# Kernel optimization log

Measured on AMD Instinct MI355X. Metric: run time of the kernel, lower is better.

The kernel has to match this reference:

```python
import jax, jax.numpy as jnp
import numpy as np

N = 20000
M = 32          # max_neighbors
IN_DIM = 256
OUT_DIM = 256
H = 4           # num_heads
D = OUT_DIM // H  # head_dim = 64
LN_EPS = 1e-5
NEG_INF = -1.0e9


def setup_inputs() -> dict:
    key = jax.random.key(0)
    ks = jax.random.split(key, 6)
    h = jax.random.normal(ks[0], (N, IN_DIM), dtype=jnp.float32)
    neighbor_idx = jax.random.randint(ks[1], (N, M), 0, N, dtype=jnp.int32)
    neighbor_mask = jax.random.randint(ks[2], (N, M), 0, 2, dtype=jnp.int32)
    # parameters (xavier-ish scaling)
    W = jax.random.normal(ks[3], (IN_DIM, OUT_DIM), dtype=jnp.float32) / np.sqrt(IN_DIM)
    a_l = jax.random.normal(ks[4], (H, D), dtype=jnp.float32) / np.sqrt(D)
    a_r = jax.random.normal(ks[5], (H, D), dtype=jnp.float32) / np.sqrt(D)
    ln_gamma = jnp.ones((OUT_DIM,), dtype=jnp.float32)
    ln_beta = jnp.zeros((OUT_DIM,), dtype=jnp.float32)
    return {"h": h, "neighbor_idx": neighbor_idx, "neighbor_mask": neighbor_mask,
            "W": W, "a_l": a_l, "a_r": a_r, "ln_gamma": ln_gamma, "ln_beta": ln_beta}


def reference(h, neighbor_idx, neighbor_mask, W, a_l, a_r, ln_gamma, ln_beta):
    h_proj = h @ W                                   # [N, OUT_DIM]
    h_heads = h_proj.reshape(N, H, D)                # [N, H, D]
    # per-node score halves; gathering scalars instead of full features for er
    el = jnp.einsum('nhd,hd->nh', h_heads, a_l)      # [N, H]
    er_node = jnp.einsum('nhd,hd->nh', h_heads, a_r) # [N, H]
    er = er_node[neighbor_idx]                       # [N, M, H]
    e = jax.nn.leaky_relu(el[:, None, :] + er, negative_slope=0.2)  # [N, M, H]
    e = jnp.where(neighbor_mask[:, :, None] == 0, NEG_INF, e)
    alpha = jax.nn.softmax(e, axis=1)                # softmax over neighbors
    neigh_h = h_heads[neighbor_idx]                  # [N, M, H, D]
    out_heads = jnp.einsum('nmh,nmhd->nhd', alpha, neigh_h)
    H_cat = out_heads.reshape(N, OUT_DIM)
    res = h_proj                                     # in_dim == out_dim -> res_proj is None
    out = jax.nn.gelu(H_cat + res, approximate=False)
    # LayerNorm over last dim
    mu = jnp.mean(out, axis=-1, keepdims=True)
    var = jnp.var(out, axis=-1, keepdims=True)
    out = (out - mu) * jax.lax.rsqrt(var + LN_EPS) * ln_gamma + ln_beta
    return out
```

## Files before the change

### kernel.cpp

```cpp
#include <hip/hip_runtime.h>
#include <math.h>

#define N_NODES 20000
#define M_NEI   32
#define DIM     256
#define H_HEADS 4
#define D_HEAD  64
#define LN_EPS  1e-5f
#define NEG_INF -1.0e9f
#define APAD    264

using short8  = __attribute__((ext_vector_type(8))) short;
using short4v = __attribute__((ext_vector_type(4))) short;
using floatx4 = __attribute__((ext_vector_type(4))) float;
using floatx2 = __attribute__((ext_vector_type(2))) float;
using uintx4  = __attribute__((ext_vector_type(4))) unsigned int;

__device__ __forceinline__ float bf2f(unsigned short u) {
    union { unsigned int i; float f; } c; c.i = ((unsigned int)u) << 16; return c.f;
}
__device__ __forceinline__ float u2f(unsigned int i) {
    union { unsigned int i; float f; } c; c.i = i; return c.f;
}
__device__ __forceinline__ unsigned short f2bf(float f) {
    union { float f; unsigned int i; } c; c.f = f;
    unsigned int x = c.i;
    x += 0x7fffu + ((x >> 16) & 1u);
    return (unsigned short)(x >> 16);
}
__device__ __forceinline__ bool in_is_fp32(const void* gamma) {
    return *(const unsigned int*)gamma == 0x3F800000u;
}

__global__ void k_prep(const void* __restrict__ W, const void* __restrict__ gamma,
                       const int* __restrict__ nidx, const int* __restrict__ nmask,
                       unsigned short* __restrict__ Wt, int* __restrict__ pidx) {
    const int b = blockIdx.x;
    const int t = threadIdx.x;
    if (b < DIM) {
        const bool f32 = in_is_fp32(gamma);
        float w = f32 ? ((const float*)W)[(size_t)t * DIM + b]
                      : bf2f(((const unsigned short*)W)[(size_t)t * DIM + b]);
        Wt[(size_t)b * DIM + t] = f2bf(w);
    } else {
        const int i = (b - DIM) * 256 + t;
        const int idx = nidx[i];
        const int msk = nmask[i];
        pidx[i] = idx | (msk ? (int)0x80000000 : 0);
    }
}

__global__ __launch_bounds__(256) void k_gemm(const void* __restrict__ A,
                                              const void* __restrict__ gamma,
                                              const unsigned short* __restrict__ Bt,
                                              const void* __restrict__ al,
                                              const void* __restrict__ ar,
                                              unsigned short* __restrict__ hp_h,
                                              float* __restrict__ el_h,
                                              float* __restrict__ er_h) {
    __shared__ unsigned short sA[16][APAD];
    const bool f32 = in_is_fp32(gamma);
    const int t    = threadIdx.x;
    const int m0   = blockIdx.x * 16;

    #pragma unroll
    for (int it = 0; it < 2; ++it) {
        int chunk = it * 256 + t;
        int row   = chunk >> 5;
        int c16   = chunk & 31;
        short8 v;
        if (!f32) {
            v = *(const short8*)((const unsigned short*)A + (size_t)(m0 + row) * DIM + c16 * 8);
        } else {
            const float* ap = (const float*)A + (size_t)(m0 + row) * DIM + c16 * 8;
            #pragma unroll
            for (int j = 0; j < 8; ++j) v[j] = (short)f2bf(ap[j]);
        }
        *(short8*)&sA[row][c16 * 8] = v;
    }
    __syncthreads();

    const int hd   = t >> 6;
    const int lane = t & 63;
    const int r    = lane & 15;
    const int quad = lane >> 4;
    const int n0   = hd * 64;

    floatx4 acc[4];
    #pragma unroll
    for (int c = 0; c < 4; ++c) acc[c] = (floatx4){0.f, 0.f, 0.f, 0.f};

    #pragma unroll
    for (int k0 = 0; k0 < DIM; k0 += 32) {
        short8 a = *(const short8*)&sA[r][k0 + quad * 8];
        #pragma unroll
        for (int c = 0; c < 4; ++c) {
            short8 b = *(const short8*)(Bt + (size_t)(n0 + c * 16 + r) * DIM + k0 + quad * 8);
            acc[c] = __builtin_amdgcn_mfma_f32_16x16x32_bf16(a, b, acc[c], 0, 0, 0);
        }
    }

    float alv[4], arv[4];
    #pragma unroll
    for (int c = 0; c < 4; ++c) {
        int col = n0 + c * 16 + r;
        if (f32) { alv[c] = ((const float*)al)[col]; arv[c] = ((const float*)ar)[col]; }
        else     { alv[c] = bf2f(((const unsigned short*)al)[col]);
                   arv[c] = bf2f(((const unsigned short*)ar)[col]); }
    }

    #pragma unroll
    for (int rr = 0; rr < 4; ++rr) {
        const int row = m0 + quad * 4 + rr;
        float sl = 0.f, sr = 0.f;
        #pragma unroll
        for (int c = 0; c < 4; ++c) {
            float v = acc[c][rr];
            sl += v * alv[c];
            sr += v * arv[c];
            hp_h[((size_t)hd * N_NODES + row) * D_HEAD + c * 16 + r] = f2bf(v);
        }
        #pragma unroll
        for (int off = 1; off < 16; off <<= 1) {
            sl += __shfl_xor(sl, off);
            sr += __shfl_xor(sr, off);
        }
        if (r == 0) {
            el_h[(size_t)hd * N_NODES + row] = sl;
            er_h[(size_t)hd * N_NODES + row] = sr;
        }
    }
}

__global__ __launch_bounds__(256) void k_attn_h(const int* __restrict__ pidx,
                                                const unsigned short* __restrict__ hp_h,
                                                const float* __restrict__ el_h,
                                                const float* __restrict__ er_h,
                                                unsigned short* __restrict__ out_h) {
    __shared__ int2 s_oa[32][33];

    const int hd  = blockIdx.x & 3;
    const int nb0 = (blockIdx.x >> 2) * 32;
    const int t   = threadIdx.x;

    {
        const int m   = t & 31;
        const int sub = t >> 5;
        #pragma unroll
        for (int it = 0; it < 4; ++it) {
            const int nl = it * 8 + sub;
            const int n  = nb0 + nl;
            const int v  = pidx[(size_t)n * M_NEI + m];
            const int idx = v & 0x7fffffff;
            float e = el_h[(size_t)hd * N_NODES + n] + er_h[(size_t)hd * N_NODES + idx];
            e = (e > 0.f) ? e : 0.2f * e;
            e = (v < 0) ? e : NEG_INF;
            float mx = e;
            #pragma unroll
            for (int off = 1; off < 32; off <<= 1) mx = fmaxf(mx, __shfl_xor(mx, off, 32));
            float a = expf(e - mx);
            float sm = a;
            #pragma unroll
            for (int off = 1; off < 32; off <<= 1) sm += __shfl_xor(sm, off, 32);
            int2 oa;
            oa.x = idx * (D_HEAD * 2);
            union { float f; int i; } c; c.f = a / sm;
            oa.y = c.i;
            s_oa[nl][m] = oa;
        }
    }
    __syncthreads();

    const int wave = t >> 6;
    const int lane = t & 63;
    const int g    = lane >> 3;
    const int s    = lane & 7;
    const int nl   = wave * 8 + g;
    const int n    = nb0 + nl;
    const char* tbl = (const char*)hp_h + (size_t)hd * N_NODES * (D_HEAD * 2) + s * 16;

    floatx2 acc[4];
    #pragma unroll
    for (int j = 0; j < 4; ++j) acc[j] = (floatx2){0.f, 0.f};

    #pragma unroll
    for (int m = 0; m < M_NEI; ++m) {
        const int2  oa = s_oa[nl][m];
        const float aa = u2f((unsigned int)oa.y);
        uintx4 u = *(const uintx4*)(tbl + oa.x);
        #pragma unroll
        for (int j = 0; j < 4; ++j) {
            floatx2 f = { u2f(u[j] << 16), u2f(u[j] & 0xffff0000u) };
            acc[j] += (floatx2){aa, aa} * f;
        }
    }

    {
        uintx4 u = *(const uintx4*)((const char*)hp_h
                     + ((size_t)hd * N_NODES + n) * (D_HEAD * 2) + s * 16);
        #pragma unroll
        for (int j = 0; j < 4; ++j) {
            floatx2 f = { u2f(u[j] << 16), u2f(u[j] & 0xffff0000u) };
            acc[j] += f;
        }
    }

    short8 o;
    #pragma unroll
    for (int j = 0; j < 4; ++j) {
        o[2 * j]     = (short)f2bf(acc[j][0]);
        o[2 * j + 1] = (short)f2bf(acc[j][1]);
    }
    *(short8*)(out_h + ((size_t)hd * N_NODES + n) * D_HEAD + s * 8) = o;
}

__global__ __launch_bounds__(256) void k_final(const unsigned short* __restrict__ out_h,
                                               const void* __restrict__ gamma,
                                               const void* __restrict__ beta,
                                               void* __restrict__ out) {
    const bool f32 = in_is_fp32(gamma);
    const int wave = threadIdx.x >> 6;
    const int lane = threadIdx.x & 63;
    const int n    = blockIdx.x * 4 + wave;
    const int h    = lane >> 4;
    const int d0   = (lane & 15) * 4;

    const size_t off = ((size_t)h * N_NODES + n) * D_HEAD + d0;
    short4v ov = *(const short4v*)(out_h + off);

    float x[4], s1 = 0.f, s2 = 0.f;
    #pragma unroll
    for (int i = 0; i < 4; ++i) {
        float xi = bf2f((unsigned short)ov[i]);
        xi = 0.5f * xi * (1.f + erff(xi * 0.70710678118654752f));
        x[i] = xi;
        s1 += xi;
        s2 += xi * xi;
    }
    #pragma unroll
    for (int offv = 1; offv < 64; offv <<= 1) {
        s1 += __shfl_xor(s1, offv);
        s2 += __shfl_xor(s2, offv);
    }
    const float mu  = s1 * (1.f / 256.f);
    float var = s2 * (1.f / 256.f) - mu * mu;
    var = fmaxf(var, 0.f);
    const float inv = rsqrtf(var + LN_EPS);

    if (f32) {
        const float* gp = (const float*)gamma + lane * 4;
        const float* bp = (const float*)beta  + lane * 4;
        float* op = (float*)out + (size_t)n * DIM + lane * 4;
        #pragma unroll
        for (int i = 0; i < 4; ++i)
            op[i] = (x[i] - mu) * inv * gp[i] + bp[i];
    } else {
        const unsigned short* gp = (const unsigned short*)gamma + lane * 4;
        const unsigned short* bp = (const unsigned short*)beta  + lane * 4;
        short4v o;
        #pragma unroll
        for (int i = 0; i < 4; ++i) {
            float y = (x[i] - mu) * inv * bf2f(gp[i]) + bf2f(bp[i]);
            o[i] = (short)f2bf(y);
        }
        *(short4v*)((unsigned short*)out + (size_t)n * DIM + lane * 4) = o;
    }
}

extern "C" void kernel_launch(void* const* d_in, const int* in_sizes, int n_in,
                              void* d_out, int out_size, void* d_ws, size_t ws_size,
                              hipStream_t stream) {
    const void* h     = d_in[0];
    const int*  nidx  = (const int*)d_in[1];
    const int*  nmask = (const int*)d_in[2];
    const void* W     = d_in[3];
    const void* al    = d_in[4];
    const void* ar    = d_in[5];
    const void* gamma = d_in[6];
    const void* beta  = d_in[7];

    unsigned short* Wt    = (unsigned short*)d_ws;
    unsigned short* hp_h  = (unsigned short*)((char*)d_ws + 131072);
    unsigned short* out_h = (unsigned short*)((char*)d_ws + 10371072);
    float* el_h = (float*)((char*)d_ws + 20611072);
    float* er_h = (float*)((char*)d_ws + 20931072);
    int*   pidx = (int*)((char*)d_ws + 21251072);

    k_prep<<<DIM + (N_NODES * M_NEI) / 256, 256, 0, stream>>>(W, gamma, nidx, nmask, Wt, pidx);
    k_gemm<<<N_NODES / 16, 256, 0, stream>>>(h, gamma, Wt, al, ar, hp_h, el_h, er_h);
    k_attn_h<<<H_HEADS * (N_NODES / 32), 256, 0, stream>>>(pidx, hp_h, el_h, er_h, out_h);
    k_final<<<N_NODES / 4, 256, 0, stream>>>(out_h, gamma, beta, d_out);
}
```

Before: 140.7 us.

## Drop packed index precompute and double GEMM row tile per block

The prep kernel no longer packs neighbor index and mask into one int array. The attention kernel now reads idx and mask directly, which removes a 2.56MB write plus a read-back but adds a second load stream per neighbor. The GEMM kernel now handles 32 rows per block with two MFMA row fragments sharing each B load, halving block count and B traffic at the cost of more registers and fewer blocks (625).

```diff
diff --git a/kernel.cpp b/kernel.cpp
--- a/kernel.cpp
+++ b/kernel.cpp
@@ -33,21 +33,13 @@
 }
 
 __global__ void k_prep(const void* __restrict__ W, const void* __restrict__ gamma,
-                       const int* __restrict__ nidx, const int* __restrict__ nmask,
-                       unsigned short* __restrict__ Wt, int* __restrict__ pidx) {
-    const int b = blockIdx.x;
-    const int t = threadIdx.x;
-    if (b < DIM) {
-        const bool f32 = in_is_fp32(gamma);
-        float w = f32 ? ((const float*)W)[(size_t)t * DIM + b]
-                      : bf2f(((const unsigned short*)W)[(size_t)t * DIM + b]);
-        Wt[(size_t)b * DIM + t] = f2bf(w);
-    } else {
-        const int i = (b - DIM) * 256 + t;
-        const int idx = nidx[i];
-        const int msk = nmask[i];
-        pidx[i] = idx | (msk ? (int)0x80000000 : 0);
-    }
+                       unsigned short* __restrict__ Wt) {
+    const bool f32 = in_is_fp32(gamma);
+    const int n = blockIdx.x;
+    const int k = threadIdx.x;
+    float w = f32 ? ((const float*)W)[(size_t)k * DIM + n]
+                  : bf2f(((const unsigned short*)W)[(size_t)k * DIM + n]);
+    Wt[(size_t)n * DIM + k] = f2bf(w);
 }
 
 __global__ __launch_bounds__(256) void k_gemm(const void* __restrict__ A,
@@ -58,13 +50,13 @@
                                               unsigned short* __restrict__ hp_h,
                                               float* __restrict__ el_h,
                                               float* __restrict__ er_h) {
-    __shared__ unsigned short sA[16][APAD];
+    __shared__ unsigned short sA[32][APAD];
     const bool f32 = in_is_fp32(gamma);
     const int t    = threadIdx.x;
-    const int m0   = blockIdx.x * 16;
-
-    #pragma unroll
-    for (int it = 0; it < 2; ++it) {
+    const int m0   = blockIdx.x * 32;
+
+    #pragma unroll
+    for (int it = 0; it < 4; ++it) {
         int chunk = it * 256 + t;
         int row   = chunk >> 5;
         int c16   = chunk & 31;
@@ -86,17 +78,21 @@
     const int quad = lane >> 4;
     const int n0   = hd * 64;
 
-    floatx4 acc[4];
-    #pragma unroll
-    for (int c = 0; c < 4; ++c) acc[c] = (floatx4){0.f, 0.f, 0.f, 0.f};
+    floatx4 acc[2][4];
+    #pragma unroll
+    for (int rf = 0; rf < 2; ++rf)
+        #pragma unroll
+        for (int c = 0; c < 4; ++c) acc[rf][c] = (floatx4){0.f, 0.f, 0.f, 0.f};
 
     #pragma unroll
     for (int k0 = 0; k0 < DIM; k0 += 32) {
-        short8 a = *(const short8*)&sA[r][k0 + quad * 8];
+        short8 a0 = *(const short8*)&sA[r][k0 + quad * 8];
+        short8 a1 = *(const short8*)&sA[16 + r][k0 + quad * 8];
         #pragma unroll
         for (int c = 0; c < 4; ++c) {
             short8 b = *(const short8*)(Bt + (size_t)(n0 + c * 16 + r) * DIM + k0 + quad * 8);
-            acc[c] = __builtin_amdgcn_mfma_f32_16x16x32_bf16(a, b, acc[c], 0, 0, 0);
+            acc[0][c] = __builtin_amdgcn_mfma_f32_16x16x32_bf16(a0, b, acc[0][c], 0, 0, 0);
+            acc[1][c] = __builtin_amdgcn_mfma_f32_16x16x32_bf16(a1, b, acc[1][c], 0, 0, 0);
         }
     }
 
@@ -110,29 +106,33 @@
     }
 
     #pragma unroll
-    for (int rr = 0; rr < 4; ++rr) {
-        const int row = m0 + quad * 4 + rr;
-        float sl = 0.f, sr = 0.f;
-        #pragma unroll
-        for (int c = 0; c < 4; ++c) {
-            float v = acc[c][rr];
-            sl += v * alv[c];
-            sr += v * arv[c];
-            hp_h[((size_t)hd * N_NODES + row) * D_HEAD + c * 16 + r] = f2bf(v);
-        }
-        #pragma unroll
-        for (int off = 1; off < 16; off <<= 1) {
-            sl += __shfl_xor(sl, off);
-            sr += __shfl_xor(sr, off);
-        }
-        if (r == 0) {
-            el_h[(size_t)hd * N_NODES + row] = sl;
-            er_h[(size_t)hd * N_NODES + row] = sr;
-        }
-    }
-}
-
-__global__ __launch_bounds__(256) void k_attn_h(const int* __restrict__ pidx,
+    for (int rf = 0; rf < 2; ++rf) {
+        #pragma unroll
+        for (int rr = 0; rr < 4; ++rr) {
+            const int row = m0 + rf * 16 + quad * 4 + rr;
+            float sl = 0.f, sr = 0.f;
+            #pragma unroll
+            for (int c = 0; c < 4; ++c) {
+                float v = acc[rf][c][rr];
+                sl += v * alv[c];
+                sr += v * arv[c];
+                hp_h[((size_t)hd * N_NODES + row) * D_HEAD + c * 16 + r] = f2bf(v);
+            }
+            #pragma unroll
+            for (int off = 1; off < 16; off <<= 1) {
+                sl += __shfl_xor(sl, off);
+                sr += __shfl_xor(sr, off);
+            }
+            if (r == 0) {
+                el_h[(size_t)hd * N_NODES + row] = sl;
+                er_h[(size_t)hd * N_NODES + row] = sr;
+            }
+        }
+    }
+}
+
+__global__ __launch_bounds__(256) void k_attn_h(const int* __restrict__ nidx,
+                                                const int* __restrict__ nmask,
                                                 const unsigned short* __restrict__ hp_h,
                                                 const float* __restrict__ el_h,
                                                 const float* __restrict__ er_h,
@@ -148,13 +148,13 @@
         const int sub = t >> 5;
         #pragma unroll
         for (int it = 0; it < 4; ++it) {
-            const int nl = it * 8 + sub;
-            const int n  = nb0 + nl;
-            const int v  = pidx[(size_t)n * M_NEI + m];
-            const int idx = v & 0x7fffffff;
+            const int nl  = it * 8 + sub;
+            const int n   = nb0 + nl;
+            const int idx = nidx[(size_t)n * M_NEI + m];
+            const int msk = nmask[(size_t)n * M_NEI + m];
             float e = el_h[(size_t)hd * N_NODES + n] + er_h[(size_t)hd * N_NODES + idx];
             e = (e > 0.f) ? e : 0.2f * e;
-            e = (v < 0) ? e : NEG_INF;
+            e = msk ? e : NEG_INF;
             float mx = e;
             #pragma unroll
             for (int off = 1; off < 32; off <<= 1) mx = fmaxf(mx, __shfl_xor(mx, off, 32));
@@ -284,10 +284,9 @@
     unsigned short* out_h = (unsigned short*)((char*)d_ws + 10371072);
     float* el_h = (float*)((char*)d_ws + 20611072);
     float* er_h = (float*)((char*)d_ws + 20931072);
-    int*   pidx = (int*)((char*)d_ws + 21251072);
-
-    k_prep<<<DIM + (N_NODES * M_NEI) / 256, 256, 0, stream>>>(W, gamma, nidx, nmask, Wt, pidx);
-    k_gemm<<<N_NODES / 16, 256, 0, stream>>>(h, gamma, Wt, al, ar, hp_h, el_h, er_h);
-    k_attn_h<<<H_HEADS * (N_NODES / 32), 256, 0, stream>>>(pidx, hp_h, el_h, er_h, out_h);
+
+    k_prep<<<DIM, 256, 0, stream>>>(W, gamma, Wt);
+    k_gemm<<<N_NODES / 32, 256, 0, stream>>>(h, gamma, Wt, al, ar, hp_h, el_h, er_h);
+    k_attn_h<<<H_HEADS * (N_NODES / 32), 256, 0, stream>>>(nidx, nmask, hp_h, el_h, er_h, out_h);
     k_final<<<N_NODES / 4, 256, 0, stream>>>(out_h, gamma, beta, d_out);
 }
```

Measured after the change: 134.5 us. -4.4%, faster.
